# Performance work log

Measured on AMD Instinct MI355X. Metric: run time of the kernel, lower is better.

The kernel has to match this reference:

```python
import jax, jax.numpy as jnp
from jax import lax
import numpy as np

H = W = 2048
C = 3
KSIZE = 2
SIGMA = 2.0
ITERATIONS = 2
RADII = (256.0, 768.0)
# with max_displacement=0 all circle centers coincide, so 'close to any circle'
# reduces to distance^2 < max(radius^2)
SRADII_MAX = max(r ** 2 for r in RADII)
SCLEAN_MAX = max(max(r - KSIZE, 0.0) ** 2 for r in RADII)


def _gaussian_blur(x, sigma):
    """skimage.filters.gaussian equivalent: separable gaussian, truncate=4.0,
    mode='nearest' (edge padding), channel_axis=-1 (no blur across channels)."""
    radius = int(4.0 * sigma + 0.5)
    t = np.arange(-radius, radius + 1, dtype=np.float32)
    k = np.exp(-0.5 * (t / sigma) ** 2)
    k = (k / k.sum()).astype(np.float32)
    for axis in (0, 1):
        pad = [(0, 0)] * x.ndim
        pad[axis] = (radius, radius)
        xp = jnp.pad(x, pad, mode='edge')
        n = x.shape[axis]
        acc = jnp.zeros_like(x)
        for j in range(k.shape[0]):
            acc = acc + k[j] * lax.slice_in_dim(xp, j, j + n, axis=axis)
        x = acc
    return x


def _glass_forward(img, offsets):
    r = KSIZE
    Hv = H - 2 * r + 1  # loop range(r, H-r+1) -> H-2r+1 rows
    Wv = W - 2 * r + 1
    HWtot = H * W
    # original quirk: cx = shape[0]//2 compared against column index w,
    # cy = shape[1]//2 against row index h; identical for a square image.
    cx = H // 2
    cy = W // 2
    ys = jnp.arange(r, H - r + 1)
    xs = jnp.arange(r, W - r + 1)
    HH, WW = jnp.meshgrid(ys, xs, indexing='ij')  # (Hv, Wv)
    d2 = (cx - WW) ** 2 + (cy - HH) ** 2
    swap_mask = (d2 >= SRADII_MAX).reshape(-1)  # swap only OUTSIDE all circles
    local = ((HH - r) * Wv + (WW - r)).reshape(-1)  # raster order within loop
    lin = (HH * W + WW).reshape(-1)

    # Every read in the original swap loop comes from array_orig (never
    # updated), so the final value of each pixel equals array_orig[source]
    # where source is determined by the LAST write targeting that pixel.
    # Each loop step emits two ordered writes:
    #   array[h, w]   = orig[h_, w_]   (order = 2*raster)
    #   array[h_, w_] = orig[h, w]    (order = 2*raster + 1)
    # We replay this exactly with a scatter-max over write order.
    writes = []
    for i in range(ITERATIONS):
        dh = offsets[i, :, :, 0]
        dw = offsets[i, :, :, 1]
        lin_ = ((HH + dh) * W + (WW + dw)).reshape(-1)
        base = i * 2 * Hv * Wv
        o1 = base + 2 * local
        o2 = o1 + 1
        writes.append((lin, lin_, o1))
        writes.append((lin_, lin, o2))

    win = jnp.full((HWtot,), -1, jnp.int32)
    for tgt, src_idx, order in writes:
        win = win.at[tgt].max(jnp.where(swap_mask, order, -1))
    src = jnp.full((HWtot,), -1, jnp.int32)
    for tgt, src_idx, order in writes:
        hit = swap_mask & (order == win[tgt])
        src = src.at[tgt].max(jnp.where(hit, src_idx, -1))

    orig_flat = img.reshape(HWtot, C)
    gathered = orig_flat[jnp.maximum(src, 0)]
    swapped = jnp.where((src >= 0)[:, None], gathered, orig_flat).reshape(H, W, C)

    blurred = jnp.clip(_gaussian_blur(swapped / 255.0, SIGMA), 0.0, 1.0) * 255.0

    # restore original pixels close to the shrunken (clean) circles
    clean = d2 < SCLEAN_MAX  # (Hv, Wv)
    clean_full = jnp.zeros((H, W), bool).at[r:H - r + 1, r:W - r + 1].set(clean)
    return jnp.where(clean_full[:, :, None], img, blurred)


def setup_inputs() -> dict:
    key = jax.random.key(0)
    k1, k2 = jax.random.split(key)
    img = jax.random.uniform(k1, (H, W, C), jnp.float32) * 255.0
    offsets = jax.random.randint(
        k2, (ITERATIONS, H - 2 * KSIZE + 1, W - 2 * KSIZE + 1, 2),
        -KSIZE, KSIZE, dtype=jnp.int32)
    return {"img": img, "offsets": offsets}


def reference(img, offsets):
    return _glass_forward(img, offsets)
```

## Files before the change

kernel.cpp:

```cpp
#include <hip/hip_runtime.h>
#include <hip/hip_fp16.h>

#define Hh 2048
#define Ww 2048
#define HW (2048 * 2048)
constexpr int REG = 2045;
constexpr int RBASE = 2 * 2045 * 2045;
constexpr int SWAP_D2 = 589824;
constexpr int CLEAN_D2 = 586756;

__device__ __constant__ float GK[17] = {
    6.691628e-05f, 4.363490e-04f, 2.215963e-03f, 8.764304e-03f,
    2.699596e-02f, 6.475994e-02f, 1.209875e-01f, 1.760358e-01f,
    1.9947466e-01f, 1.760358e-01f, 1.209875e-01f, 6.475994e-02f,
    2.699596e-02f, 8.764304e-03f, 2.215963e-03f, 4.363490e-04f,
    6.691628e-05f};

constexpr int TX = 32, TY = 8;
constexpr int HX = TX + 3, HY = TY + 3;

__global__ __launch_bounds__(256) void swap_gather(
    const float* __restrict__ img, const int* __restrict__ off,
    __half* __restrict__ A) {
  int x0 = blockIdx.x * TX, y0 = blockIdx.y * TY;
  int tx = threadIdx.x & 31, ty = threadIdx.x >> 5;
  int px = x0 + tx, py = y0 + ty;
  int plin = py * Ww + px;
  int srcoff = 0;

  int mxx = max(abs(1024 - (x0 - 1)), abs(1024 - (x0 + TX + 1)));
  int mxy = max(abs(1024 - (y0 - 1)), abs(1024 - (y0 + TY + 1)));
  if (mxx * mxx + mxy * mxy >= SWAP_D2) {
    __shared__ unsigned sh[HY * HX];
    for (int e = threadIdx.x; e < HY * HX; e += 256) {
      int ly = e / HX, lx = e - ly * HX;
      int qy = y0 - 1 + ly, qx = x0 - 1 + lx;
      unsigned v = 0xFFFFFFFFu;
      int dcx = 1024 - qx, dcy = 1024 - qy;
      if (qy >= 2 && qy <= 2046 && qx >= 2 && qx <= 2046 &&
          dcx * dcx + dcy * dcy >= SWAP_D2) {
        int base = ((qy - 2) * REG + (qx - 2)) * 2;
        const int2 a0 = *(const int2*)&off[base];
        const int2 a1 = *(const int2*)&off[RBASE + base];
        v = (unsigned)(a0.y + 2) | ((unsigned)(a0.x + 2) << 8) |
            ((unsigned)(a1.y + 2) << 16) | ((unsigned)(a1.x + 2) << 24);
      }
      sh[e] = v;
    }
    __syncthreads();

    unsigned w[4][4];
#pragma unroll
    for (int dyi = 0; dyi < 4; ++dyi)
#pragma unroll
      for (int dxi = 0; dxi < 4; ++dxi)
        w[dyi][dxi] = sh[(ty + dyi) * HX + (tx + dxi)];

#define CANDC(dyi, dxi) ((unsigned)((1 - (dxi)) + 2) | ((unsigned)((1 - (dyi)) + 2) << 8))
#define OFFC(dyi, dxi) (-(1 - (dyi)) * Ww - (1 - (dxi)))
#define CAND0(dyi, dxi) \
  if ((w[dyi][dxi] & 0xFFFFu) == CANDC(dyi, dxi)) srcoff = OFFC(dyi, dxi);
#define CAND1(dyi, dxi) \
  if ((w[dyi][dxi] >> 16) == CANDC(dyi, dxi)) srcoff = OFFC(dyi, dxi);

    CAND0(0, 0) CAND0(0, 1) CAND0(0, 2) CAND0(0, 3)
    CAND0(1, 0) CAND0(1, 1) CAND0(1, 2) CAND0(1, 3)
    CAND0(2, 0) CAND0(2, 1) CAND0(2, 2) CAND0(2, 3)
    CAND0(3, 0) CAND0(3, 1) CAND0(3, 2) CAND0(3, 3)
    CAND1(0, 0) CAND1(0, 1) CAND1(0, 2) CAND1(0, 3)
    CAND1(1, 0)
    {
      unsigned wc = w[1][1];
      if ((wc >> 24) != 0xFFu) {
        int dh1 = (int)((wc >> 24) & 0xFFu) - 2;
        int dw1 = (int)((wc >> 16) & 0xFFu) - 2;
        srcoff = dh1 * Ww + dw1;
      }
    }
    CAND1(1, 1) CAND1(1, 2) CAND1(1, 3)
    CAND1(2, 0) CAND1(2, 1) CAND1(2, 2) CAND1(2, 3)
    CAND1(3, 0) CAND1(3, 1) CAND1(3, 2) CAND1(3, 3)
#undef CANDC
#undef OFFC
#undef CAND0
#undef CAND1
  }

  int src = plin + srcoff;
  float r = img[src * 3 + 0];
  float g = img[src * 3 + 1];
  float b = img[src * 3 + 2];
  A[plin] = __float2half(r);
  A[HW + plin] = __float2half(g);
  A[2 * HW + plin] = __float2half(b);
}

constexpr int YPT = 16;
__global__ __launch_bounds__(256) void vblur(const __half* __restrict__ A,
                                             __half* __restrict__ B) {
  int b = blockIdx.x;
  int xcd = b & 7, r = b >> 3;
  int ystrip = (xcd << 4) | (r & 15);
  int rem = r >> 4;
  int xb = rem & 1, c = rem >> 1;
  int x0 = (xb * 256 + threadIdx.x) * 4;
  int y0 = ystrip * YPT;
  const __half* Ap = A + (size_t)c * HW;
  __half* Bp = B + (size_t)c * HW;

  float acc[YPT][4];
#pragma unroll
  for (int k = 0; k < YPT; ++k)
#pragma unroll
    for (int q = 0; q < 4; ++q) acc[k][q] = 0.f;

#pragma unroll
  for (int j = 0; j < YPT + 16; ++j) {
    int ys = y0 - 8 + j;
    ys = ys < 0 ? 0 : (ys > Hh - 1 ? Hh - 1 : ys);
    uint2 raw = *(const uint2*)&Ap[(size_t)ys * Ww + x0];
    __half2 h01 = *(__half2*)&raw.x;
    __half2 h23 = *(__half2*)&raw.y;
    float2 v01 = __half22float2(h01);
    float2 v23 = __half22float2(h23);
#pragma unroll
    for (int k = 0; k < YPT; ++k) {
      int t = j - k;
      if (t >= 0 && t <= 16) {
        float gk = GK[t];
        acc[k][0] += gk * v01.x;
        acc[k][1] += gk * v01.y;
        acc[k][2] += gk * v23.x;
        acc[k][3] += gk * v23.y;
      }
    }
  }
#pragma unroll
  for (int k = 0; k < YPT; ++k) {
    uint2 o;
    __half2 h01 = __float22half2_rn(make_float2(acc[k][0], acc[k][1]));
    __half2 h23 = __float22half2_rn(make_float2(acc[k][2], acc[k][3]));
    o.x = *(unsigned*)&h01;
    o.y = *(unsigned*)&h23;
    *(uint2*)&Bp[(size_t)(y0 + k) * Ww + x0] = o;
  }
}

__global__ __launch_bounds__(256) void hblur_compose(
    const __half* __restrict__ B, const float* __restrict__ img,
    float* __restrict__ out) {
  __shared__ float tile[528 + 1];
  int tid = threadIdx.x;
  int xs = blockIdx.x * 512;
  int y = blockIdx.y;
  float br[3][2];

  for (int c = 0; c < 3; ++c) {
    const __half* Bp = B + (size_t)c * HW + (size_t)y * Ww;
    __syncthreads();
    for (int e = tid; e < 264; e += 256) {
      int xg = xs - 8 + 2 * e;
      float2 v;
      if (xg >= 0 && xg + 1 <= Ww - 1) {
        __half2 h = *(const __half2*)&Bp[xg];
        v = __half22float2(h);
      } else {
        int xlo = xg < 0 ? 0 : (xg > Ww - 1 ? Ww - 1 : xg);
        int xhi = xg + 1 < 0 ? 0 : (xg + 1 > Ww - 1 ? Ww - 1 : xg + 1);
        v = make_float2(__half2float(Bp[xlo]), __half2float(Bp[xhi]));
      }
      *(float2*)&tile[2 * e] = v;
    }
    __syncthreads();
    float f[19];
#pragma unroll
    for (int j = 0; j < 19; ++j) f[j] = tile[2 * tid + j];
    float s0 = 0.f, s1 = 0.f;
#pragma unroll
    for (int j = 0; j < 17; ++j) {
      s0 += GK[j] * f[j];
      s1 += GK[j] * f[j + 1];
    }
    br[c][0] = s0;
    br[c][1] = s1;
  }

  int x = xs + 2 * tid;
#pragma unroll
  for (int u = 0; u < 2; ++u) {
    int xu = x + u;
    int dx = 1024 - xu, dy = 1024 - y;
    bool clean = (xu >= 2 && xu <= 2046 && y >= 2 && y <= 2046 &&
                  dx * dx + dy * dy < CLEAN_D2);
    int p3 = (y * Ww + xu) * 3;
    if (clean) {
      out[p3 + 0] = img[p3 + 0];
      out[p3 + 1] = img[p3 + 1];
      out[p3 + 2] = img[p3 + 2];
    } else {
#pragma unroll
      for (int c = 0; c < 3; ++c) {
        float v = br[c][u];
        v = v < 0.f ? 0.f : (v > 255.f ? 255.f : v);
        out[p3 + c] = v;
      }
    }
  }
}

extern "C" void kernel_launch(void* const* d_in, const int* in_sizes, int n_in,
                              void* d_out, int out_size, void* d_ws,
                              size_t ws_size, hipStream_t stream) {
  const float* img = (const float*)d_in[0];
  const int* off = (const int*)d_in[1];
  float* out = (float*)d_out;

  __half* A = (__half*)d_ws;
  __half* Bp = A + (size_t)3 * HW;

  swap_gather<<<dim3(Ww / TX, Hh / TY), 256, 0, stream>>>(img, off, A);
  vblur<<<768, 256, 0, stream>>>(A, Bp);
  hblur_compose<<<dim3(Ww / 512, Hh), 256, 0, stream>>>(Bp, img, out);
}
```

Measured before the change: 179.5 us.

## Skip blur work inside clean circle and vectorize swap-gather per four pixels

Swap_gather now returns early for tiles whose final output is overwritten by the clean region. Tiles fully inside the no-swap circle take a vectorized copy path, and each thread handles four pixels with wider tiles and vector stores. Vblur skips column strips whose outputs only feed clean pixels. Hblur_compose copies the original image directly for row segments fully inside the clean circle. The aim is to cut the wasted memory traffic and compute in the large central region, at the cost of more complex bounds reasoning where a conservative margin error could corrupt pixels near the circle edge.

```diff
diff --git a/kernel.cpp b/kernel.cpp
--- a/kernel.cpp
+++ b/kernel.cpp
@@ -8,6 +8,7 @@
 constexpr int RBASE = 2 * 2045 * 2045;
 constexpr int SWAP_D2 = 589824;
 constexpr int CLEAN_D2 = 586756;
+constexpr int DEAD_D2 = 568516;
 
 __device__ __constant__ float GK[17] = {
     6.691628e-05f, 4.363490e-04f, 2.215963e-03f, 8.764304e-03f,
@@ -16,83 +17,117 @@
     2.699596e-02f, 8.764304e-03f, 2.215963e-03f, 4.363490e-04f,
     6.691628e-05f};
 
-constexpr int TX = 32, TY = 8;
+struct F3 { float x, y, z; };
+
+constexpr int TX = 64, TY = 16;
 constexpr int HX = TX + 3, HY = TY + 3;
 
 __global__ __launch_bounds__(256) void swap_gather(
     const float* __restrict__ img, const int* __restrict__ off,
     __half* __restrict__ A) {
   int x0 = blockIdx.x * TX, y0 = blockIdx.y * TY;
-  int tx = threadIdx.x & 31, ty = threadIdx.x >> 5;
-  int px = x0 + tx, py = y0 + ty;
+
+  int sdx = max(abs(1024 - x0), abs(1024 - (x0 + TX - 1)));
+  int sdy = max(abs(1024 - y0), abs(1024 - (y0 + TY - 1)));
+  if (sdx * sdx + sdy * sdy <= DEAD_D2) return;
+
+  int tx4 = (threadIdx.x & 15) * 4, ty = threadIdx.x >> 4;
+  int px = x0 + tx4, py = y0 + ty;
   int plin = py * Ww + px;
-  int srcoff = 0;
 
   int mxx = max(abs(1024 - (x0 - 1)), abs(1024 - (x0 + TX + 1)));
   int mxy = max(abs(1024 - (y0 - 1)), abs(1024 - (y0 + TY + 1)));
-  if (mxx * mxx + mxy * mxy >= SWAP_D2) {
-    __shared__ unsigned sh[HY * HX];
-    for (int e = threadIdx.x; e < HY * HX; e += 256) {
-      int ly = e / HX, lx = e - ly * HX;
-      int qy = y0 - 1 + ly, qx = x0 - 1 + lx;
-      unsigned v = 0xFFFFFFFFu;
-      int dcx = 1024 - qx, dcy = 1024 - qy;
-      if (qy >= 2 && qy <= 2046 && qx >= 2 && qx <= 2046 &&
-          dcx * dcx + dcy * dcy >= SWAP_D2) {
-        int base = ((qy - 2) * REG + (qx - 2)) * 2;
-        const int2 a0 = *(const int2*)&off[base];
-        const int2 a1 = *(const int2*)&off[RBASE + base];
-        v = (unsigned)(a0.y + 2) | ((unsigned)(a0.x + 2) << 8) |
-            ((unsigned)(a1.y + 2) << 16) | ((unsigned)(a1.x + 2) << 24);
-      }
-      sh[e] = v;
-    }
-    __syncthreads();
-
-    unsigned w[4][4];
-#pragma unroll
-    for (int dyi = 0; dyi < 4; ++dyi)
-#pragma unroll
-      for (int dxi = 0; dxi < 4; ++dxi)
-        w[dyi][dxi] = sh[(ty + dyi) * HX + (tx + dxi)];
-
-#define CANDC(dyi, dxi) ((unsigned)((1 - (dxi)) + 2) | ((unsigned)((1 - (dyi)) + 2) << 8))
+  if (mxx * mxx + mxy * mxy < SWAP_D2) {
+    const float4 c0 = *(const float4*)(img + (size_t)plin * 3);
+    const float4 c1 = *(const float4*)(img + (size_t)plin * 3 + 4);
+    const float4 c2 = *(const float4*)(img + (size_t)plin * 3 + 8);
+    float v[12] = {c0.x, c0.y, c0.z, c0.w, c1.x, c1.y, c1.z, c1.w,
+                   c2.x, c2.y, c2.z, c2.w};
+#pragma unroll
+    for (int c = 0; c < 3; ++c) {
+      __half2 h01 = __float22half2_rn(make_float2(v[c], v[3 + c]));
+      __half2 h23 = __float22half2_rn(make_float2(v[6 + c], v[9 + c]));
+      uint2 o = make_uint2(*(unsigned*)&h01, *(unsigned*)&h23);
+      *(uint2*)&A[(size_t)c * HW + plin] = o;
+    }
+    return;
+  }
+
+  __shared__ unsigned sh[HY * HX];
+  for (int e = threadIdx.x; e < HY * HX; e += 256) {
+    int ly = e / HX, lx = e - ly * HX;
+    int qy = y0 - 1 + ly, qx = x0 - 1 + lx;
+    unsigned v = 0xFFFFFFFFu;
+    int dcx = 1024 - qx, dcy = 1024 - qy;
+    if (qy >= 2 && qy <= 2046 && qx >= 2 && qx <= 2046 &&
+        dcx * dcx + dcy * dcy >= SWAP_D2) {
+      int base = ((qy - 2) * REG + (qx - 2)) * 2;
+      const int2 a0 = *(const int2*)&off[base];
+      const int2 a1 = *(const int2*)&off[RBASE + base];
+      v = (unsigned)(a0.y + 2) | ((unsigned)(a0.x + 2) << 8) |
+          ((unsigned)(a1.y + 2) << 16) | ((unsigned)(a1.x + 2) << 24);
+    }
+    sh[e] = v;
+  }
+  __syncthreads();
+
+  unsigned w[4][7];
+#pragma unroll
+  for (int dyi = 0; dyi < 4; ++dyi)
+#pragma unroll
+    for (int c = 0; c < 7; ++c) w[dyi][c] = sh[(ty + dyi) * HX + tx4 + c];
+
+  int so[4] = {0, 0, 0, 0};
+
+#define CANDC(dyi, dxi) \
+  ((unsigned)((1 - (dxi)) + 2) | ((unsigned)((1 - (dyi)) + 2) << 8))
 #define OFFC(dyi, dxi) (-(1 - (dyi)) * Ww - (1 - (dxi)))
-#define CAND0(dyi, dxi) \
-  if ((w[dyi][dxi] & 0xFFFFu) == CANDC(dyi, dxi)) srcoff = OFFC(dyi, dxi);
-#define CAND1(dyi, dxi) \
-  if ((w[dyi][dxi] >> 16) == CANDC(dyi, dxi)) srcoff = OFFC(dyi, dxi);
-
-    CAND0(0, 0) CAND0(0, 1) CAND0(0, 2) CAND0(0, 3)
-    CAND0(1, 0) CAND0(1, 1) CAND0(1, 2) CAND0(1, 3)
-    CAND0(2, 0) CAND0(2, 1) CAND0(2, 2) CAND0(2, 3)
-    CAND0(3, 0) CAND0(3, 1) CAND0(3, 2) CAND0(3, 3)
-    CAND1(0, 0) CAND1(0, 1) CAND1(0, 2) CAND1(0, 3)
-    CAND1(1, 0)
-    {
-      unsigned wc = w[1][1];
-      if ((wc >> 24) != 0xFFu) {
-        int dh1 = (int)((wc >> 24) & 0xFFu) - 2;
-        int dw1 = (int)((wc >> 16) & 0xFFu) - 2;
-        srcoff = dh1 * Ww + dw1;
-      }
-    }
-    CAND1(1, 1) CAND1(1, 2) CAND1(1, 3)
-    CAND1(2, 0) CAND1(2, 1) CAND1(2, 2) CAND1(2, 3)
-    CAND1(3, 0) CAND1(3, 1) CAND1(3, 2) CAND1(3, 3)
+#define C0(j, dyi, dxi) \
+  if ((w[dyi][(j) + (dxi)] & 0xFFFFu) == CANDC(dyi, dxi)) so[j] = OFFC(dyi, dxi);
+#define C1(j, dyi, dxi) \
+  if ((w[dyi][(j) + (dxi)] >> 16) == CANDC(dyi, dxi)) so[j] = OFFC(dyi, dxi);
+#define PXSEQ(j)                                                        \
+  C0(j, 0, 0) C0(j, 0, 1) C0(j, 0, 2) C0(j, 0, 3)                       \
+  C0(j, 1, 0) C0(j, 1, 1) C0(j, 1, 2) C0(j, 1, 3)                       \
+  C0(j, 2, 0) C0(j, 2, 1) C0(j, 2, 2) C0(j, 2, 3)                       \
+  C0(j, 3, 0) C0(j, 3, 1) C0(j, 3, 2) C0(j, 3, 3)                       \
+  C1(j, 0, 0) C1(j, 0, 1) C1(j, 0, 2) C1(j, 0, 3)                       \
+  C1(j, 1, 0)                                                           \
+  { unsigned wc = w[1][(j) + 1];                                        \
+    if ((wc >> 24) != 0xFFu) {                                          \
+      int dh1 = (int)((wc >> 24) & 0xFFu) - 2;                          \
+      int dw1 = (int)((wc >> 16) & 0xFFu) - 2;                          \
+      so[j] = dh1 * Ww + dw1; } }                                       \
+  C1(j, 1, 1) C1(j, 1, 2) C1(j, 1, 3)                                   \
+  C1(j, 2, 0) C1(j, 2, 1) C1(j, 2, 2) C1(j, 2, 3)                       \
+  C1(j, 3, 0) C1(j, 3, 1) C1(j, 3, 2) C1(j, 3, 3)
+
+  PXSEQ(0) PXSEQ(1) PXSEQ(2) PXSEQ(3)
 #undef CANDC
 #undef OFFC
-#undef CAND0
-#undef CAND1
-  }
-
-  int src = plin + srcoff;
-  float r = img[src * 3 + 0];
-  float g = img[src * 3 + 1];
-  float b = img[src * 3 + 2];
-  A[plin] = __float2half(r);
-  A[HW + plin] = __float2half(g);
-  A[2 * HW + plin] = __float2half(b);
+#undef C0
+#undef C1
+#undef PXSEQ
+
+  F3 g[4];
+#pragma unroll
+  for (int j = 0; j < 4; ++j)
+    g[j] = *(const F3*)(img + (size_t)(plin + j + so[j]) * 3);
+  {
+    __half2 h01 = __float22half2_rn(make_float2(g[0].x, g[1].x));
+    __half2 h23 = __float22half2_rn(make_float2(g[2].x, g[3].x));
+    *(uint2*)&A[plin] = make_uint2(*(unsigned*)&h01, *(unsigned*)&h23);
+  }
+  {
+    __half2 h01 = __float22half2_rn(make_float2(g[0].y, g[1].y));
+    __half2 h23 = __float22half2_rn(make_float2(g[2].y, g[3].y));
+    *(uint2*)&A[HW + plin] = make_uint2(*(unsigned*)&h01, *(unsigned*)&h23);
+  }
+  {
+    __half2 h01 = __float22half2_rn(make_float2(g[0].z, g[1].z));
+    __half2 h23 = __float22half2_rn(make_float2(g[2].z, g[3].z));
+    *(uint2*)&A[2 * HW + plin] = make_uint2(*(unsigned*)&h01, *(unsigned*)&h23);
+  }
 }
 
 constexpr int YPT = 16;
@@ -105,6 +140,13 @@
   int xb = rem & 1, c = rem >> 1;
   int x0 = (xb * 256 + threadIdx.x) * 4;
   int y0 = ystrip * YPT;
+
+  int adx = max(abs(1024 - x0), abs(1024 - (x0 + 3))) + 8;
+  int ady = max(abs(1024 - y0), abs(1024 - (y0 + YPT - 1)));
+  if (y0 >= 2 && y0 + YPT - 1 <= 2046 && x0 >= 10 && x0 + 3 <= 2035 &&
+      adx * adx + ady * ady < CLEAN_D2)
+    return;
+
   const __half* Ap = A + (size_t)c * HW;
   __half* Bp = B + (size_t)c * HW;
 
@@ -153,8 +195,18 @@
   int tid = threadIdx.x;
   int xs = blockIdx.x * 512;
   int y = blockIdx.y;
+
+  int mdx = max(abs(1024 - xs), abs(1024 - (xs + 511)));
+  int mdy = abs(1024 - y);
+  if (xs >= 2 && xs + 511 <= 2046 && y >= 2 && y <= 2046 &&
+      mdx * mdx + mdy * mdy < CLEAN_D2) {
+    const float4* s4 = (const float4*)(img + (size_t)(y * Ww + xs) * 3);
+    float4* d4 = (float4*)(out + (size_t)(y * Ww + xs) * 3);
+    for (int e = tid; e < 384; e += 256) d4[e] = s4[e];
+    return;
+  }
+
   float br[3][2];
-
   for (int c = 0; c < 3; ++c) {
     const __half* Bp = B + (size_t)c * HW + (size_t)y * Ww;
     __syncthreads();
```

Measured after the change: 187.9 us. 4.7% more time.
